# Kernel tuning notes

Hardware: AMD Instinct MI355X
Metric: run time of the kernel (lower is better)

Reference implementation:

```python
import jax, jax.numpy as jnp
import numpy as np

N_NODES = 100000
N_EDGES = 1000000
IN_DIM = 64
HID = 64
OUT = 64
NEG_SLOPE = 0.2  # PyG GATConv default


def setup_inputs() -> dict:
    key = jax.random.key(0)
    ks = jax.random.split(key, 10)
    x = jax.random.normal(ks[0], (N_NODES, IN_DIM), dtype=jnp.float32)
    edge_index = jax.random.randint(ks[1], (2, N_EDGES), 0, N_NODES, dtype=jnp.int64)
    s = 1.0 / np.sqrt(IN_DIM)
    sh = 1.0 / np.sqrt(HID)
    W_src = jax.random.uniform(ks[2], (IN_DIM, HID), jnp.float32, -s, s)
    W_dst = jax.random.uniform(ks[3], (IN_DIM, HID), jnp.float32, -s, s)
    att_src = jax.random.uniform(ks[4], (HID,), jnp.float32, -sh, sh)
    att_dst = jax.random.uniform(ks[5], (HID,), jnp.float32, -sh, sh)
    bias = jnp.zeros((HID,), jnp.float32)
    W_lin = jax.random.uniform(ks[6], (HID, OUT), jnp.float32, -sh, sh)
    b_lin = jax.random.uniform(ks[7], (OUT,), jnp.float32, -sh, sh)
    return {"x": x, "edge_index": edge_index, "W_src": W_src, "W_dst": W_dst,
            "att_src": att_src, "att_dst": att_dst, "bias": bias,
            "W_lin": W_lin, "b_lin": b_lin}


def reference(x, edge_index, W_src, W_dst, att_src, att_dst, bias, W_lin, b_lin):
    src, tgt = edge_index[0], edge_index[1]
    # Bias-free linear projections (PyG GATConv with tuple in_channels)
    h_src = x @ W_src                      # [N, HID]
    h_dst = x @ W_dst                      # [N, HID]
    a_src = h_src @ att_src                # [N]
    a_dst = h_dst @ att_dst                # [N]
    # Per-edge attention logits: LeakyReLU(a_src[j] + a_dst[i])
    e = a_src[src] + a_dst[tgt]            # [E]
    e = jnp.where(e > 0, e, NEG_SLOPE * e)
    # Segment-softmax over incoming edges of each target node
    seg_max = jax.ops.segment_max(e, tgt, num_segments=N_NODES)  # [N]
    expw = jnp.exp(e - seg_max[tgt])                             # [E]
    denom = jax.ops.segment_sum(expw, tgt, num_segments=N_NODES)  # [N]
    alpha = expw / (denom[tgt] + 1e-16)                          # [E]
    # Scatter-aggregate weighted source features
    msgs = alpha[:, None] * h_src[src]                           # [E, HID]
    out = jax.ops.segment_sum(msgs, tgt, num_segments=N_NODES)   # [N, HID]
    out = out + bias
    # Final linear + ReLU
    return jax.nn.relu(out @ W_lin + b_lin)
```

## Files before the change

### kernel.cpp

```cpp
#include <hip/hip_runtime.h>
#include <hip/hip_fp16.h>
#include <math.h>

#define HID 64
#define CBITS 6
#define CSZ 64
#define MAXB 2048
#define CAP 832
#define PB 896
#define MSB 256
#define XSTR 17

__device__ __forceinline__ float4 f4fma(float a, const float4 b, float4 c) {
    c.x = fmaf(a, b.x, c.x); c.y = fmaf(a, b.y, c.y);
    c.z = fmaf(a, b.z, c.z); c.w = fmaf(a, b.w, c.w);
    return c;
}

__global__ void init_kernel(const float* __restrict__ W_dst,
                            const float* __restrict__ att_dst,
                            float* __restrict__ vdst,
                            int* __restrict__ gcursor, int nbc) {
    if (blockIdx.x == 0 && threadIdx.x < HID) {
        int k = threadIdx.x;
        float acc = 0.0f;
#pragma unroll 8
        for (int h = 0; h < HID; ++h) acc = fmaf(W_dst[k * HID + h], att_dst[h], acc);
        vdst[k] = acc;
    }
    int stride = gridDim.x * blockDim.x;
    for (int i = blockIdx.x * blockDim.x + threadIdx.x; i < nbc; i += stride)
        gcursor[i] = i * CAP;
}

__global__ void __launch_bounds__(256)
mid_kernel(const float* __restrict__ x,
           const float* __restrict__ W_src,
           const float* __restrict__ att_src,
           const float* __restrict__ vdst,
           __half* __restrict__ h_half,
           float* __restrict__ a_src,
           float* __restrict__ a_dst, int N,
           const int* __restrict__ src, const int* __restrict__ tgt,
           int* __restrict__ gcursor, int* __restrict__ rec, int E, int nbc) {
    __shared__ __align__(16) char smraw[25600];
    const int t = threadIdx.x;

    if (blockIdx.x < PB) {
        float4* Ws4  = (float4*)smraw;
        float4* att4 = Ws4 + HID * 16;
        float4* vd4  = att4 + 16;
        float4* xsl  = vd4 + 16;

        for (int i = t; i < HID * 16; i += 256) Ws4[i] = ((const float4*)W_src)[i];
        if (t < 16) {
            att4[t] = ((const float4*)att_src)[t];
            vd4[t]  = ((const float4*)vdst)[t];
        }
        __syncthreads();

        const int w    = t >> 6;
        const int lane = t & 63;
        const int g    = lane >> 4;
        const int s    = lane & 15;
        float4* slice = xsl + w * (8 * XSTR);
        const float4* x4 = (const float4*)x;
        uint2* h2 = (uint2*)h_half;
        const float4 zf4 = make_float4(0, 0, 0, 0);

        for (int base = blockIdx.x * 32; base < N; base += PB * 32) {
            const int nodeW = base + w * 8;
#pragma unroll
            for (int u = 0; u < 2; ++u) {
                int f = lane + u * 64;
                int row = f >> 4, col = f & 15;
                int node = nodeW + row;
                slice[row * XSTR + col] =
                    (node < N) ? x4[(long long)node * 16 + col] : zf4;
            }

            const float4* xr0 = slice + g * XSTR;
            const float4* xr1 = slice + (g + 4) * XSTR;

            float4 acc0 = zf4, acc1 = zf4;
#pragma unroll 4
            for (int kk = 0; kk < 16; ++kk) {
                float4 xv0 = xr0[kk];
                float4 xv1 = xr1[kk];
                float4 w0 = Ws4[(4 * kk + 0) * 16 + s];
                float4 w1 = Ws4[(4 * kk + 1) * 16 + s];
                float4 w2 = Ws4[(4 * kk + 2) * 16 + s];
                float4 w3 = Ws4[(4 * kk + 3) * 16 + s];
                acc0 = f4fma(xv0.x, w0, acc0);
                acc1 = f4fma(xv1.x, w0, acc1);
                acc0 = f4fma(xv0.y, w1, acc0);
                acc1 = f4fma(xv1.y, w1, acc1);
                acc0 = f4fma(xv0.z, w2, acc0);
                acc1 = f4fma(xv1.z, w2, acc1);
                acc0 = f4fma(xv0.w, w3, acc0);
                acc1 = f4fma(xv1.w, w3, acc1);
            }

            float4 av = att4[s], qv = vd4[s];
            float p0 = acc0.x * av.x + acc0.y * av.y + acc0.z * av.z + acc0.w * av.w;
            float p1 = acc1.x * av.x + acc1.y * av.y + acc1.z * av.z + acc1.w * av.w;
            float4 xq0 = xr0[s];
            float4 xq1 = xr1[s];
            float q0 = xq0.x * qv.x + xq0.y * qv.y + xq0.z * qv.z + xq0.w * qv.w;
            float q1 = xq1.x * qv.x + xq1.y * qv.y + xq1.z * qv.z + xq1.w * qv.w;
#pragma unroll
            for (int off = 1; off < 16; off <<= 1) {
                p0 += __shfl_xor(p0, off, 64);
                p1 += __shfl_xor(p1, off, 64);
                q0 += __shfl_xor(q0, off, 64);
                q1 += __shfl_xor(q1, off, 64);
            }

            int n0 = nodeW + g, n1 = nodeW + g + 4;
            if (n0 < N) {
                __half2 lo = __float22half2_rn(make_float2(acc0.x, acc0.y));
                __half2 hi = __float22half2_rn(make_float2(acc0.z, acc0.w));
                uint2 pk; pk.x = *(unsigned*)&lo; pk.y = *(unsigned*)&hi;
                h2[(long long)n0 * 16 + s] = pk;
                if (s == 0) { a_src[n0] = p0; a_dst[n0] = q0; }
            }
            if (n1 < N) {
                __half2 lo = __float22half2_rn(make_float2(acc1.x, acc1.y));
                __half2 hi = __float22half2_rn(make_float2(acc1.z, acc1.w));
                uint2 pk; pk.x = *(unsigned*)&lo; pk.y = *(unsigned*)&hi;
                h2[(long long)n1 * 16 + s] = pk;
                if (s == 0) { a_src[n1] = p1; a_dst[n1] = q1; }
            }
        }
    } else {
        int* lh  = (int*)smraw;
        int* tch = lh + nbc;
        const int bid = blockIdx.x - PB;

        for (int i = t; i < nbc; i += 256) lh[i] = 0;
        __syncthreads();
        int chunk = (E + MSB - 1) / MSB;
        int e0 = bid * chunk;
        int e1 = min(E, e0 + chunk);
        int len = e1 - e0;
        for (int i = t; i < len; i += 256) {
            int tg = tgt[e0 + i];
            tch[i] = tg;
            atomicAdd(&lh[tg >> CBITS], 1);
        }
        __syncthreads();
        for (int i = t; i < nbc; i += 256)
            if (lh[i]) lh[i] = atomicAdd(&gcursor[i], lh[i]);
        __syncthreads();
        for (int i = t; i < len; i += 256) {
            int tg = tch[i];
            int s = src[e0 + i];
            int bi = tg >> CBITS;
            int pos = atomicAdd(&lh[bi], 1);
            if (pos < (bi + 1) * CAP)
                rec[pos] = (s << CBITS) | (tg & (CSZ - 1));
        }
    }
}

__global__ void __launch_bounds__(256)
sort_gather_kernel(const int* __restrict__ gcursor, const int* __restrict__ rec,
                   const __half* __restrict__ h_half,
                   const float* __restrict__ a_src, const float* __restrict__ a_dst,
                   const float* __restrict__ bias,
                   const float* __restrict__ W_lin, const float* __restrict__ b_lin,
                   float* __restrict__ out, int N) {
    __shared__ float4 Wl4[HID * 16];
    __shared__ float4 bs4[16], bl4[16];
    __shared__ int ssort[CAP];
    __shared__ int hist[CSZ];
    __shared__ int loff[CSZ + 1];
    __shared__ int cur[CSZ];

    const int t = threadIdx.x;
    for (int i = t; i < HID * 16; i += 256) Wl4[i] = ((const float4*)W_lin)[i];
    if (t < 16) {
        bs4[t] = ((const float4*)bias)[t];
        bl4[t] = ((const float4*)b_lin)[t];
    }

    const int bk = blockIdx.x;
    const int node0 = bk << CBITS;
    const int nn = min(CSZ, N - node0);
    const int beg = bk * CAP;
    int cnt = gcursor[bk] - beg;
    if (cnt > CAP) cnt = CAP;

    if (t < CSZ) hist[t] = 0;
    __syncthreads();
    for (int j = t; j < cnt; j += 256)
        atomicAdd(&hist[rec[beg + j] & (CSZ - 1)], 1);
    __syncthreads();
    if (t < CSZ) {
        int h = hist[t];
        int v = h;
#pragma unroll
        for (int off = 1; off < CSZ; off <<= 1) {
            int u = __shfl_up(v, off, 64);
            if (t >= off) v += u;
        }
        loff[t] = v - h;
        cur[t]  = v - h;
        if (t == CSZ - 1) loff[CSZ] = v;
    }
    __syncthreads();
    for (int j = t; j < cnt; j += 256) {
        int r = rec[beg + j];
        int pos = atomicAdd(&cur[r & (CSZ - 1)], 1);
        ssort[pos] = r >> CBITS;
    }
    __syncthreads();

    const int lane = t & 63;
    const int w = t >> 6;
    const int g = lane >> 4;
    const int s = lane & 15;
    const int gbase = g << 4;
    const uint2* h2 = (const uint2*)h_half;
    float4* out4 = (float4*)out;

#pragma unroll 1
    for (int r2 = 0; r2 < 4; ++r2) {
        int nloc = w * 16 + r2 * 4 + g;
        int n = node0 + nloc;
        bool act = (nloc < nn);
        float adn = act ? a_dst[n] : 0.0f;
        int jb = loff[nloc];
        int je = loff[nloc + 1];

        float4 acc = make_float4(0, 0, 0, 0);
        float dsum = 0.0f;
        int j = jb;
        for (; j + 4 <= je; j += 4) {
            int s0 = ssort[j], s1 = ssort[j + 1], s2 = ssort[j + 2], s3 = ssort[j + 3];
            uint2 r0 = h2[(long long)s0 * 16 + s];
            uint2 r1 = h2[(long long)s1 * 16 + s];
            uint2 r2v = h2[(long long)s2 * 16 + s];
            uint2 r3 = h2[(long long)s3 * 16 + s];
            float v0 = a_src[s0] + adn, v1 = a_src[s1] + adn;
            float v2 = a_src[s2] + adn, v3 = a_src[s3] + adn;
            v0 = (v0 > 0.0f) ? v0 : 0.2f * v0;
            v1 = (v1 > 0.0f) ? v1 : 0.2f * v1;
            v2 = (v2 > 0.0f) ? v2 : 0.2f * v2;
            v3 = (v3 > 0.0f) ? v3 : 0.2f * v3;
            float w0 = __expf(v0), w1 = __expf(v1);
            float w2 = __expf(v2), w3 = __expf(v3);
            dsum += (w0 + w1) + (w2 + w3);
            float2 f0a = __half22float2(*(const __half2*)&r0.x);
            float2 f0b = __half22float2(*(const __half2*)&r0.y);
            float2 f1a = __half22float2(*(const __half2*)&r1.x);
            float2 f1b = __half22float2(*(const __half2*)&r1.y);
            float2 f2a = __half22float2(*(const __half2*)&r2v.x);
            float2 f2b = __half22float2(*(const __half2*)&r2v.y);
            float2 f3a = __half22float2(*(const __half2*)&r3.x);
            float2 f3b = __half22float2(*(const __half2*)&r3.y);
            acc.x = fmaf(w0, f0a.x, fmaf(w1, f1a.x, fmaf(w2, f2a.x, fmaf(w3, f3a.x, acc.x))));
            acc.y = fmaf(w0, f0a.y, fmaf(w1, f1a.y, fmaf(w2, f2a.y, fmaf(w3, f3a.y, acc.y))));
            acc.z = fmaf(w0, f0b.x, fmaf(w1, f1b.x, fmaf(w2, f2b.x, fmaf(w3, f3b.x, acc.z))));
            acc.w = fmaf(w0, f0b.y, fmaf(w1, f1b.y, fmaf(w2, f2b.y, fmaf(w3, f3b.y, acc.w))));
        }
        for (; j < je; ++j) {
            int s0 = ssort[j];
            uint2 r0 = h2[(long long)s0 * 16 + s];
            float v0 = a_src[s0] + adn;
            v0 = (v0 > 0.0f) ? v0 : 0.2f * v0;
            float w0 = __expf(v0);
            dsum += w0;
            float2 f0a = __half22float2(*(const __half2*)&r0.x);
            float2 f0b = __half22float2(*(const __half2*)&r0.y);
            acc.x = fmaf(w0, f0a.x, acc.x);
            acc.y = fmaf(w0, f0a.y, acc.y);
            acc.z = fmaf(w0, f0b.x, acc.z);
            acc.w = fmaf(w0, f0b.y, acc.w);
        }

        float inv = 1.0f / (dsum + 1e-16f);
        float4 bsv = bs4[s];
        float4 r;
        r.x = fmaf(acc.x, inv, bsv.x);
        r.y = fmaf(acc.y, inv, bsv.y);
        r.z = fmaf(acc.z, inv, bsv.z);
        r.w = fmaf(acc.w, inv, bsv.w);

        float4 o = bl4[s];
#pragma unroll 4
        for (int ks = 0; ks < 16; ++ks) {
            float rx = __shfl(r.x, gbase + ks, 64);
            float ry = __shfl(r.y, gbase + ks, 64);
            float rz = __shfl(r.z, gbase + ks, 64);
            float rw = __shfl(r.w, gbase + ks, 64);
            o = f4fma(rx, Wl4[(4 * ks + 0) * 16 + s], o);
            o = f4fma(ry, Wl4[(4 * ks + 1) * 16 + s], o);
            o = f4fma(rz, Wl4[(4 * ks + 2) * 16 + s], o);
            o = f4fma(rw, Wl4[(4 * ks + 3) * 16 + s], o);
        }

        if (act) {
            float4 res;
            res.x = o.x > 0.0f ? o.x : 0.0f;
            res.y = o.y > 0.0f ? o.y : 0.0f;
            res.z = o.z > 0.0f ? o.z : 0.0f;
            res.w = o.w > 0.0f ? o.w : 0.0f;
            out4[(long long)n * 16 + s] = res;
        }
    }
}

extern "C" void kernel_launch(void* const* d_in, const int* in_sizes, int n_in,
                              void* d_out, int out_size, void* d_ws, size_t ws_size,
                              hipStream_t stream) {
    const float* x       = (const float*)d_in[0];
    const int*   edge    = (const int*)d_in[1];
    const float* W_src   = (const float*)d_in[2];
    const float* W_dst   = (const float*)d_in[3];
    const float* att_src = (const float*)d_in[4];
    const float* att_dst = (const float*)d_in[5];
    const float* bias    = (const float*)d_in[6];
    const float* W_lin   = (const float*)d_in[7];
    const float* b_lin   = (const float*)d_in[8];
    float* out = (float*)d_out;

    const int N = in_sizes[0] / HID;
    const int E = in_sizes[1] / 2;
    const int* src = edge;
    const int* tgt = edge + E;
    const int nbc = (N + CSZ - 1) / CSZ;

    __half* h_half  = (__half*)d_ws;
    float*  a_src   = (float*)(h_half + (size_t)N * HID);
    float*  a_dst   = a_src + N;
    float*  vdst    = a_dst + N;
    int*    gcursor = (int*)(vdst + 64);
    int*    rec     = gcursor + MAXB;

    init_kernel<<<8, 256, 0, stream>>>(W_dst, att_dst, vdst, gcursor, nbc);
    mid_kernel<<<PB + MSB, 256, 0, stream>>>(x, W_src, att_src, vdst, h_half,
                                             a_src, a_dst, N,
                                             src, tgt, gcursor, rec, E, nbc);
    sort_gather_kernel<<<nbc, 256, 0, stream>>>(gcursor, rec, h_half, a_src, a_dst,
                                                bias, W_lin, b_lin, out, N);
}
```

Measured before the change: 161.2 us.

## Fuse three kernels into one cooperative persistent kernel with grid syncs

```diff
diff --git a/kernel.cpp b/kernel.cpp
--- a/kernel.cpp
+++ b/kernel.cpp
@@ -1,15 +1,17 @@
 #include <hip/hip_runtime.h>
 #include <hip/hip_fp16.h>
+#include <hip/hip_cooperative_groups.h>
 #include <math.h>
+
+namespace cg = cooperative_groups;
 
 #define HID 64
 #define CBITS 6
 #define CSZ 64
 #define MAXB 2048
 #define CAP 832
-#define PB 896
-#define MSB 256
 #define XSTR 17
+#define SMB 21504
 
 __device__ __forceinline__ float4 f4fma(float a, const float4 b, float4 c) {
     c.x = fmaf(a, b.x, c.x); c.y = fmaf(a, b.y, c.y);
@@ -17,36 +19,41 @@
     return c;
 }
 
-__global__ void init_kernel(const float* __restrict__ W_dst,
-                            const float* __restrict__ att_dst,
-                            float* __restrict__ vdst,
-                            int* __restrict__ gcursor, int nbc) {
-    if (blockIdx.x == 0 && threadIdx.x < HID) {
-        int k = threadIdx.x;
-        float acc = 0.0f;
+__global__ void __launch_bounds__(256, 7)
+fused_kernel(const float* __restrict__ x,
+             const float* __restrict__ W_src,
+             const float* __restrict__ W_dst,
+             const float* __restrict__ att_src,
+             const float* __restrict__ att_dst,
+             __half* __restrict__ h_half,
+             float* __restrict__ a_src,
+             float* __restrict__ a_dst, int N,
+             const int* __restrict__ src, const int* __restrict__ tgt,
+             int* __restrict__ gcursor, int* __restrict__ rec, int E, int nbc,
+             int PBn, float* __restrict__ vdst,
+             const float* __restrict__ bias,
+             const float* __restrict__ W_lin, const float* __restrict__ b_lin,
+             float* __restrict__ out) {
+    __shared__ __align__(16) char smraw[SMB];
+    const int t = threadIdx.x;
+    const int b = blockIdx.x;
+    const int G = gridDim.x;
+    cg::grid_group grid = cg::this_grid();
+
+    {
+        int stride = G * 256;
+        for (int i = b * 256 + t; i < nbc; i += stride) gcursor[i] = i * CAP;
+        if (b == 0 && t < HID) {
+            float acc = 0.0f;
 #pragma unroll 8
-        for (int h = 0; h < HID; ++h) acc = fmaf(W_dst[k * HID + h], att_dst[h], acc);
-        vdst[k] = acc;
+            for (int h = 0; h < HID; ++h)
+                acc = fmaf(W_dst[t * HID + h], att_dst[h], acc);
+            vdst[t] = acc;
+        }
     }
-    int stride = gridDim.x * blockDim.x;
-    for (int i = blockIdx.x * blockDim.x + threadIdx.x; i < nbc; i += stride)
-        gcursor[i] = i * CAP;
-}
-
-__global__ void __launch_bounds__(256)
-mid_kernel(const float* __restrict__ x,
-           const float* __restrict__ W_src,
-           const float* __restrict__ att_src,
-           const float* __restrict__ vdst,
-           __half* __restrict__ h_half,
-           float* __restrict__ a_src,
-           float* __restrict__ a_dst, int N,
-           const int* __restrict__ src, const int* __restrict__ tgt,
-           int* __restrict__ gcursor, int* __restrict__ rec, int E, int nbc) {
-    __shared__ __align__(16) char smraw[25600];
-    const int t = threadIdx.x;
-
-    if (blockIdx.x < PB) {
+    grid.sync();
+
+    if (b < PBn) {
         float4* Ws4  = (float4*)smraw;
         float4* att4 = Ws4 + HID * 16;
         float4* vd4  = att4 + 16;
@@ -63,51 +70,73 @@
         const int lane = t & 63;
         const int g    = lane >> 4;
         const int s    = lane & 15;
-        float4* slice = xsl + w * (8 * XSTR);
+        float4* slice = xsl + w * (4 * XSTR);
         const float4* x4 = (const float4*)x;
         uint2* h2 = (uint2*)h_half;
         const float4 zf4 = make_float4(0, 0, 0, 0);
-
-        for (int base = blockIdx.x * 32; base < N; base += PB * 32) {
+        const float4 av = att4[s], qv = vd4[s];
+
+        for (int base = b * 32; base < N; base += PBn * 32) {
             const int nodeW = base + w * 8;
-#pragma unroll
-            for (int u = 0; u < 2; ++u) {
-                int f = lane + u * 64;
-                int row = f >> 4, col = f & 15;
+            {
+                int row = lane >> 4, col = lane & 15;
                 int node = nodeW + row;
                 slice[row * XSTR + col] =
                     (node < N) ? x4[(long long)node * 16 + col] : zf4;
             }
-
-            const float4* xr0 = slice + g * XSTR;
-            const float4* xr1 = slice + (g + 4) * XSTR;
-
-            float4 acc0 = zf4, acc1 = zf4;
+            const float4* xr = slice + g * XSTR;
+            float4 acc0 = zf4;
 #pragma unroll 4
             for (int kk = 0; kk < 16; ++kk) {
-                float4 xv0 = xr0[kk];
-                float4 xv1 = xr1[kk];
+                float4 xv = xr[kk];
                 float4 w0 = Ws4[(4 * kk + 0) * 16 + s];
                 float4 w1 = Ws4[(4 * kk + 1) * 16 + s];
                 float4 w2 = Ws4[(4 * kk + 2) * 16 + s];
                 float4 w3 = Ws4[(4 * kk + 3) * 16 + s];
-                acc0 = f4fma(xv0.x, w0, acc0);
-                acc1 = f4fma(xv1.x, w0, acc1);
-                acc0 = f4fma(xv0.y, w1, acc0);
-                acc1 = f4fma(xv1.y, w1, acc1);
-                acc0 = f4fma(xv0.z, w2, acc0);
-                acc1 = f4fma(xv1.z, w2, acc1);
-                acc0 = f4fma(xv0.w, w3, acc0);
-                acc1 = f4fma(xv1.w, w3, acc1);
-            }
-
-            float4 av = att4[s], qv = vd4[s];
+                acc0 = f4fma(xv.x, w0, acc0);
+                acc0 = f4fma(xv.y, w1, acc0);
+                acc0 = f4fma(xv.z, w2, acc0);
+                acc0 = f4fma(xv.w, w3, acc0);
+            }
             float p0 = acc0.x * av.x + acc0.y * av.y + acc0.z * av.z + acc0.w * av.w;
+            float4 xq0 = xr[s];
+            float q0 = xq0.x * qv.x + xq0.y * qv.y + xq0.z * qv.z + xq0.w * qv.w;
+            int n0 = nodeW + g;
+            if (n0 < N) {
+                __half2 lo = __float22half2_rn(make_float2(acc0.x, acc0.y));
+                __half2 hi = __float22half2_rn(make_float2(acc0.z, acc0.w));
+                uint2 pk; pk.x = *(unsigned*)&lo; pk.y = *(unsigned*)&hi;
+                h2[(long long)n0 * 16 + s] = pk;
+            }
+            {
+                int row = lane >> 4, col = lane & 15;
+                int node = nodeW + 4 + row;
+                slice[row * XSTR + col] =
+                    (node < N) ? x4[(long long)node * 16 + col] : zf4;
+            }
+            float4 acc1 = zf4;
+#pragma unroll 4
+            for (int kk = 0; kk < 16; ++kk) {
+                float4 xv = xr[kk];
+                float4 w0 = Ws4[(4 * kk + 0) * 16 + s];
+                float4 w1 = Ws4[(4 * kk + 1) * 16 + s];
+                float4 w2 = Ws4[(4 * kk + 2) * 16 + s];
+                float4 w3 = Ws4[(4 * kk + 3) * 16 + s];
+                acc1 = f4fma(xv.x, w0, acc1);
+                acc1 = f4fma(xv.y, w1, acc1);
+                acc1 = f4fma(xv.z, w2, acc1);
+                acc1 = f4fma(xv.w, w3, acc1);
+            }
             float p1 = acc1.x * av.x + acc1.y * av.y + acc1.z * av.z + acc1.w * av.w;
-            float4 xq0 = xr0[s];
-            float4 xq1 = xr1[s];
-            float q0 = xq0.x * qv.x + xq0.y * qv.y + xq0.z * qv.z + xq0.w * qv.w;
+            float4 xq1 = xr[s];
             float q1 = xq1.x * qv.x + xq1.y * qv.y + xq1.z * qv.z + xq1.w * qv.w;
+            int n1 = nodeW + g + 4;
+            if (n1 < N) {
+                __half2 lo = __float22half2_rn(make_float2(acc1.x, acc1.y));
+                __half2 hi = __float22half2_rn(make_float2(acc1.z, acc1.w));
+                uint2 pk; pk.x = *(unsigned*)&lo; pk.y = *(unsigned*)&hi;
+                h2[(long long)n1 * 16 + s] = pk;
+            }
 #pragma unroll
             for (int off = 1; off < 16; off <<= 1) {
                 p0 += __shfl_xor(p0, off, 64);
@@ -115,198 +144,179 @@
                 q0 += __shfl_xor(q0, off, 64);
                 q1 += __shfl_xor(q1, off, 64);
             }
-
-            int n0 = nodeW + g, n1 = nodeW + g + 4;
-            if (n0 < N) {
-                __half2 lo = __float22half2_rn(make_float2(acc0.x, acc0.y));
-                __half2 hi = __float22half2_rn(make_float2(acc0.z, acc0.w));
-                uint2 pk; pk.x = *(unsigned*)&lo; pk.y = *(unsigned*)&hi;
-                h2[(long long)n0 * 16 + s] = pk;
-                if (s == 0) { a_src[n0] = p0; a_dst[n0] = q0; }
-            }
-            if (n1 < N) {
-                __half2 lo = __float22half2_rn(make_float2(acc1.x, acc1.y));
-                __half2 hi = __float22half2_rn(make_float2(acc1.z, acc1.w));
-                uint2 pk; pk.x = *(unsigned*)&lo; pk.y = *(unsigned*)&hi;
-                h2[(long long)n1 * 16 + s] = pk;
-                if (s == 0) { a_src[n1] = p1; a_dst[n1] = q1; }
+            if (s == 0) {
+                if (n0 < N) { a_src[n0] = p0; a_dst[n0] = q0; }
+                if (n1 < N) { a_src[n1] = p1; a_dst[n1] = q1; }
             }
         }
     } else {
-        int* lh  = (int*)smraw;
-        int* tch = lh + nbc;
-        const int bid = blockIdx.x - PB;
+        int* lh = (int*)smraw;
+        const int bid = b - PBn;
+        const int MSBn = G - PBn;
 
         for (int i = t; i < nbc; i += 256) lh[i] = 0;
         __syncthreads();
-        int chunk = (E + MSB - 1) / MSB;
+        int chunk = (E + MSBn - 1) / MSBn;
         int e0 = bid * chunk;
         int e1 = min(E, e0 + chunk);
-        int len = e1 - e0;
-        for (int i = t; i < len; i += 256) {
-            int tg = tgt[e0 + i];
-            tch[i] = tg;
-            atomicAdd(&lh[tg >> CBITS], 1);
-        }
+        for (int e = e0 + t; e < e1; e += 256)
+            atomicAdd(&lh[tgt[e] >> CBITS], 1);
         __syncthreads();
         for (int i = t; i < nbc; i += 256)
             if (lh[i]) lh[i] = atomicAdd(&gcursor[i], lh[i]);
         __syncthreads();
-        for (int i = t; i < len; i += 256) {
-            int tg = tch[i];
-            int s = src[e0 + i];
+        for (int e = e0 + t; e < e1; e += 256) {
+            int sv = src[e], tg = tgt[e];
             int bi = tg >> CBITS;
             int pos = atomicAdd(&lh[bi], 1);
             if (pos < (bi + 1) * CAP)
-                rec[pos] = (s << CBITS) | (tg & (CSZ - 1));
+                rec[pos] = (sv << CBITS) | (tg & (CSZ - 1));
         }
     }
-}
-
-__global__ void __launch_bounds__(256)
-sort_gather_kernel(const int* __restrict__ gcursor, const int* __restrict__ rec,
-                   const __half* __restrict__ h_half,
-                   const float* __restrict__ a_src, const float* __restrict__ a_dst,
-                   const float* __restrict__ bias,
-                   const float* __restrict__ W_lin, const float* __restrict__ b_lin,
-                   float* __restrict__ out, int N) {
-    __shared__ float4 Wl4[HID * 16];
-    __shared__ float4 bs4[16], bl4[16];
-    __shared__ int ssort[CAP];
-    __shared__ int hist[CSZ];
-    __shared__ int loff[CSZ + 1];
-    __shared__ int cur[CSZ];
-
-    const int t = threadIdx.x;
-    for (int i = t; i < HID * 16; i += 256) Wl4[i] = ((const float4*)W_lin)[i];
-    if (t < 16) {
-        bs4[t] = ((const float4*)bias)[t];
-        bl4[t] = ((const float4*)b_lin)[t];
-    }
-
-    const int bk = blockIdx.x;
-    const int node0 = bk << CBITS;
-    const int nn = min(CSZ, N - node0);
-    const int beg = bk * CAP;
-    int cnt = gcursor[bk] - beg;
-    if (cnt > CAP) cnt = CAP;
-
-    if (t < CSZ) hist[t] = 0;
-    __syncthreads();
-    for (int j = t; j < cnt; j += 256)
-        atomicAdd(&hist[rec[beg + j] & (CSZ - 1)], 1);
-    __syncthreads();
-    if (t < CSZ) {
-        int h = hist[t];
-        int v = h;
+
+    grid.sync();
+
+    {
+        float4* Wl4 = (float4*)smraw;
+        float4* bs4 = Wl4 + HID * 16;
+        float4* bl4 = bs4 + 16;
+        int* ssort  = (int*)(bl4 + 16);
+        int* hist   = ssort + CAP;
+        int* loff   = hist + CSZ;
+        int* cur    = loff + CSZ + 1;
+
+        for (int i = t; i < HID * 16; i += 256) Wl4[i] = ((const float4*)W_lin)[i];
+        if (t < 16) {
+            bs4[t] = ((const float4*)bias)[t];
+            bl4[t] = ((const float4*)b_lin)[t];
+        }
+
+        const int lane = t & 63;
+        const int w = t >> 6;
+        const int g = lane >> 4;
+        const int s = lane & 15;
+        const int gbase = g << 4;
+        const uint2* h2 = (const uint2*)h_half;
+        float4* out4 = (float4*)out;
+
+        for (int bk = b; bk < nbc; bk += G) {
+            const int node0 = bk << CBITS;
+            const int nn = min(CSZ, N - node0);
+            const int beg = bk * CAP;
+            int cnt = gcursor[bk] - beg;
+            if (cnt > CAP) cnt = CAP;
+
+            if (t < CSZ) hist[t] = 0;
+            __syncthreads();
+            for (int j = t; j < cnt; j += 256)
+                atomicAdd(&hist[rec[beg + j] & (CSZ - 1)], 1);
+            __syncthreads();
+            if (t < CSZ) {
+                int h = hist[t];
+                int v = h;
 #pragma unroll
-        for (int off = 1; off < CSZ; off <<= 1) {
-            int u = __shfl_up(v, off, 64);
-            if (t >= off) v += u;
-        }
-        loff[t] = v - h;
-        cur[t]  = v - h;
-        if (t == CSZ - 1) loff[CSZ] = v;
-    }
-    __syncthreads();
-    for (int j = t; j < cnt; j += 256) {
-        int r = rec[beg + j];
-        int pos = atomicAdd(&cur[r & (CSZ - 1)], 1);
-        ssort[pos] = r >> CBITS;
-    }
-    __syncthreads();
-
-    const int lane = t & 63;
-    const int w = t >> 6;
-    const int g = lane >> 4;
-    const int s = lane & 15;
-    const int gbase = g << 4;
-    const uint2* h2 = (const uint2*)h_half;
-    float4* out4 = (float4*)out;
+                for (int off = 1; off < CSZ; off <<= 1) {
+                    int u = __shfl_up(v, off, 64);
+                    if (t >= off) v += u;
+                }
+                loff[t] = v - h;
+                cur[t]  = v - h;
+                if (t == CSZ - 1) loff[CSZ] = v;
+            }
+            __syncthreads();
+            for (int j = t; j < cnt; j += 256) {
+                int r = rec[beg + j];
+                int pos = atomicAdd(&cur[r & (CSZ - 1)], 1);
+                ssort[pos] = r >> CBITS;
+            }
+            __syncthreads();
 
 #pragma unroll 1
-    for (int r2 = 0; r2 < 4; ++r2) {
-        int nloc = w * 16 + r2 * 4 + g;
-        int n = node0 + nloc;
-        bool act = (nloc < nn);
-        float adn = act ? a_dst[n] : 0.0f;
-        int jb = loff[nloc];
-        int je = loff[nloc + 1];
-
-        float4 acc = make_float4(0, 0, 0, 0);
-        float dsum = 0.0f;
-        int j = jb;
-        for (; j + 4 <= je; j += 4) {
-            int s0 = ssort[j], s1 = ssort[j + 1], s2 = ssort[j + 2], s3 = ssort[j + 3];
-            uint2 r0 = h2[(long long)s0 * 16 + s];
-            uint2 r1 = h2[(long long)s1 * 16 + s];
-            uint2 r2v = h2[(long long)s2 * 16 + s];
-            uint2 r3 = h2[(long long)s3 * 16 + s];
-            float v0 = a_src[s0] + adn, v1 = a_src[s1] + adn;
-            float v2 = a_src[s2] + adn, v3 = a_src[s3] + adn;
-            v0 = (v0 > 0.0f) ? v0 : 0.2f * v0;
-            v1 = (v1 > 0.0f) ? v1 : 0.2f * v1;
-            v2 = (v2 > 0.0f) ? v2 : 0.2f * v2;
-            v3 = (v3 > 0.0f) ? v3 : 0.2f * v3;
-            float w0 = __expf(v0), w1 = __expf(v1);
-            float w2 = __expf(v2), w3 = __expf(v3);
-            dsum += (w0 + w1) + (w2 + w3);
-            float2 f0a = __half22float2(*(const __half2*)&r0.x);
-            float2 f0b = __half22float2(*(const __half2*)&r0.y);
-            float2 f1a = __half22float2(*(const __half2*)&r1.x);
-            float2 f1b = __half22float2(*(const __half2*)&r1.y);
-            float2 f2a = __half22float2(*(const __half2*)&r2v.x);
-            float2 f2b = __half22float2(*(const __half2*)&r2v.y);
-            float2 f3a = __half22float2(*(const __half2*)&r3.x);
-            float2 f3b = __half22float2(*(const __half2*)&r3.y);
-            acc.x = fmaf(w0, f0a.x, fmaf(w1, f1a.x, fmaf(w2, f2a.x, fmaf(w3, f3a.x, acc.x))));
-            acc.y = fmaf(w0, f0a.y, fmaf(w1, f1a.y, fmaf(w2, f2a.y, fmaf(w3, f3a.y, acc.y))));
-            acc.z = fmaf(w0, f0b.x, fmaf(w1, f1b.x, fmaf(w2, f2b.x, fmaf(w3, f3b.x, acc.z))));
-            acc.w = fmaf(w0, f0b.y, fmaf(w1, f1b.y, fmaf(w2, f2b.y, fmaf(w3, f3b.y, acc.w))));
-        }
-        for (; j < je; ++j) {
-            int s0 = ssort[j];
-            uint2 r0 = h2[(long long)s0 * 16 + s];
-            float v0 = a_src[s0] + adn;
-            v0 = (v0 > 0.0f) ? v0 : 0.2f * v0;
-            float w0 = __expf(v0);
-            dsum += w0;
-            float2 f0a = __half22float2(*(const __half2*)&r0.x);
-            float2 f0b = __half22float2(*(const __half2*)&r0.y);
-            acc.x = fmaf(w0, f0a.x, acc.x);
-            acc.y = fmaf(w0, f0a.y, acc.y);
-            acc.z = fmaf(w0, f0b.x, acc.z);
-            acc.w = fmaf(w0, f0b.y, acc.w);
-        }
-
-        float inv = 1.0f / (dsum + 1e-16f);
-        float4 bsv = bs4[s];
-        float4 r;
-        r.x = fmaf(acc.x, inv, bsv.x);
-        r.y = fmaf(acc.y, inv, bsv.y);
-        r.z = fmaf(acc.z, inv, bsv.z);
-        r.w = fmaf(acc.w, inv, bsv.w);
-
-        float4 o = bl4[s];
+            for (int r2 = 0; r2 < 4; ++r2) {
+                int nloc = w * 16 + r2 * 4 + g;
+                int n = node0 + nloc;
+                bool act = (nloc < nn);
+                float adn = act ? a_dst[n] : 0.0f;
+                int jb = loff[nloc];
+                int je = loff[nloc + 1];
+
+                float4 acc = make_float4(0, 0, 0, 0);
+                float dsum = 0.0f;
+                int j = jb;
+                for (; j + 4 <= je; j += 4) {
+                    int s0 = ssort[j], s1 = ssort[j + 1];
+                    int s2 = ssort[j + 2], s3 = ssort[j + 3];
+                    uint2 r0 = h2[(long long)s0 * 16 + s];
+                    uint2 r1 = h2[(long long)s1 * 16 + s];
+                    uint2 r2v = h2[(long long)s2 * 16 + s];
+                    uint2 r3 = h2[(long long)s3 * 16 + s];
+                    float v0 = a_src[s0] + adn, v1 = a_src[s1] + adn;
+                    float v2 = a_src[s2] + adn, v3 = a_src[s3] + adn;
+                    v0 = (v0 > 0.0f) ? v0 : 0.2f * v0;
+                    v1 = (v1 > 0.0f) ? v1 : 0.2f * v1;
+                    v2 = (v2 > 0.0f) ? v2 : 0.2f * v2;
+                    v3 = (v3 > 0.0f) ? v3 : 0.2f * v3;
+                    float w0 = __expf(v0), w1 = __expf(v1);
+                    float w2 = __expf(v2), w3 = __expf(v3);
+                    dsum += (w0 + w1) + (w2 + w3);
+                    float2 f0a = __half22float2(*(const __half2*)&r0.x);
+                    float2 f0b = __half22float2(*(const __half2*)&r0.y);
+                    float2 f1a = __half22float2(*(const __half2*)&r1.x);
+                    float2 f1b = __half22float2(*(const __half2*)&r1.y);
+                    float2 f2a = __half22float2(*(const __half2*)&r2v.x);
+                    float2 f2b = __half22float2(*(const __half2*)&r2v.y);
+                    float2 f3a = __half22float2(*(const __half2*)&r3.x);
+                    float2 f3b = __half22float2(*(const __half2*)&r3.y);
+                    acc.x = fmaf(w0, f0a.x, fmaf(w1, f1a.x, fmaf(w2, f2a.x, fmaf(w3, f3a.x, acc.x))));
+                    acc.y = fmaf(w0, f0a.y, fmaf(w1, f1a.y, fmaf(w2, f2a.y, fmaf(w3, f3a.y, acc.y))));
+                    acc.z = fmaf(w0, f0b.x, fmaf(w1, f1b.x, fmaf(w2, f2b.x, fmaf(w3, f3b.x, acc.z))));
+                    acc.w = fmaf(w0, f0b.y, fmaf(w1, f1b.y, fmaf(w2, f2b.y, fmaf(w3, f3b.y, acc.w))));
+                }
+                for (; j < je; ++j) {
+                    int s0 = ssort[j];
+                    uint2 r0 = h2[(long long)s0 * 16 + s];
+                    float v0 = a_src[s0] + adn;
+                    v0 = (v0 > 0.0f) ? v0 : 0.2f * v0;
+                    float w0 = __expf(v0);
+                    dsum += w0;
+                    float2 f0a = __half22float2(*(const __half2*)&r0.x);
+                    float2 f0b = __half22float2(*(const __half2*)&r0.y);
+                    acc.x = fmaf(w0, f0a.x, acc.x);
+                    acc.y = fmaf(w0, f0a.y, acc.y);
+                    acc.z = fmaf(w0, f0b.x, acc.z);
+                    acc.w = fmaf(w0, f0b.y, acc.w);
+                }
+
+                float inv = 1.0f / (dsum + 1e-16f);
+                float4 bsv = bs4[s];
+                float4 r;
+                r.x = fmaf(acc.x, inv, bsv.x);
+                r.y = fmaf(acc.y, inv, bsv.y);
+                r.z = fmaf(acc.z, inv, bsv.z);
+                r.w = fmaf(acc.w, inv, bsv.w);
+
+                float4 o = bl4[s];
 #pragma unroll 4
-        for (int ks = 0; ks < 16; ++ks) {
-            float rx = __shfl(r.x, gbase + ks, 64);
-            float ry = __shfl(r.y, gbase + ks, 64);
-            float rz = __shfl(r.z, gbase + ks, 64);
-            float rw = __shfl(r.w, gbase + ks, 64);
-            o = f4fma(rx, Wl4[(4 * ks + 0) * 16 + s], o);
-            o = f4fma(ry, Wl4[(4 * ks + 1) * 16 + s], o);
-            o = f4fma(rz, Wl4[(4 * ks + 2) * 16 + s], o);
-            o = f4fma(rw, Wl4[(4 * ks + 3) * 16 + s], o);
-        }
-
-        if (act) {
-            float4 res;
-            res.x = o.x > 0.0f ? o.x : 0.0f;
-            res.y = o.y > 0.0f ? o.y : 0.0f;
-            res.z = o.z > 0.0f ? o.z : 0.0f;
-            res.w = o.w > 0.0f ? o.w : 0.0f;
-            out4[(long long)n * 16 + s] = res;
+                for (int ks = 0; ks < 16; ++ks) {
+                    float rx = __shfl(r.x, gbase + ks, 64);
+                    float ry = __shfl(r.y, gbase + ks, 64);
+                    float rz = __shfl(r.z, gbase + ks, 64);
+                    float rw = __shfl(r.w, gbase + ks, 64);
+                    o = f4fma(rx, Wl4[(4 * ks + 0) * 16 + s], o);
+                    o = f4fma(ry, Wl4[(4 * ks + 1) * 16 + s], o);
+                    o = f4fma(rz, Wl4[(4 * ks + 2) * 16 + s], o);
+                    o = f4fma(rw, Wl4[(4 * ks + 3) * 16 + s], o);
+                }
+
+                if (act) {
+                    float4 res;
+                    res.x = o.x > 0.0f ? o.x : 0.0f;
+                    res.y = o.y > 0.0f ? o.y : 0.0f;
+                    res.z = o.z > 0.0f ? o.z : 0.0f;
+                    res.w = o.w > 0.0f ? o.w : 0.0f;
+                    out4[(long long)n * 16 + s] = res;
+                }
+            }
         }
     }
 }
@@ -325,11 +335,11 @@
     const float* b_lin   = (const float*)d_in[8];
     float* out = (float*)d_out;
 
-    const int N = in_sizes[0] / HID;
-    const int E = in_sizes[1] / 2;
+    int N = in_sizes[0] / HID;
+    int E = in_sizes[1] / 2;
     const int* src = edge;
     const int* tgt = edge + E;
-    const int nbc = (N + CSZ - 1) / CSZ;
+    int nbc = (N + CSZ - 1) / CSZ;
 
     __half* h_half  = (__half*)d_ws;
     float*  a_src   = (float*)(h_half + (size_t)N * HID);
@@ -338,10 +348,20 @@
     int*    gcursor = (int*)(vdst + 64);
     int*    rec     = gcursor + MAXB;
 
-    init_kernel<<<8, 256, 0, stream>>>(W_dst, att_dst, vdst, gcursor, nbc);
-    mid_kernel<<<PB + MSB, 256, 0, stream>>>(x, W_src, att_src, vdst, h_half,
-                                             a_src, a_dst, N,
-                                             src, tgt, gcursor, rec, E, nbc);
-    sort_gather_kernel<<<nbc, 256, 0, stream>>>(gcursor, rec, h_half, a_src, a_dst,
-                                                bias, W_lin, b_lin, out, N);
+    static int blocksPerCU = -1;
+    if (blocksPerCU < 0) {
+        hipError_t err = hipOccupancyMaxActiveBlocksPerMultiprocessor(
+            &blocksPerCU, fused_kernel, 256, 0);
+        if (err != hipSuccess || blocksPerCU < 1) blocksPerCU = 4;
+    }
+    int G = blocksPerCU * 256;
+    if (G > nbc) G = nbc;
+    int PBn = (G * 4) / 5;
+
+    void* args[] = {&x, &W_src, &W_dst, &att_src, &att_dst,
+                    &h_half, &a_src, &a_dst, &N, &src, &tgt,
+                    &gcursor, &rec, &E, &nbc, &PBn, &vdst,
+                    &bias, &W_lin, &b_lin, &out};
+    hipLaunchCooperativeKernel((void*)fused_kernel, dim3(G), dim3(256),
+                               args, 0, stream);
 }
```

Result: slower. 347.4 us (+115.5%).
